# Kernel optimization log

Hardware: AMD Instinct MI355X
Metric: run time of the kernel (lower is better)

The kernel has to match this reference:

```python
import jax, jax.numpy as jnp
import numpy as np

N = 4096      # num_nodes (also node feature dim)
E = 32768     # num_edges
EMB = 8       # embedding_dim


def setup_inputs() -> dict:
    key = jax.random.key(0)
    ks = jax.random.split(key, 12)
    s = lambda fan_in: 1.0 / np.sqrt(fan_in)
    return {
        "x": jax.random.normal(ks[0], (N, N), dtype=jnp.float32),
        "edge_index": jax.random.randint(ks[1], (2, E), 0, N, dtype=jnp.int64),
        "edge_weight": jax.random.uniform(ks[2], (E,), dtype=jnp.float32),
        # GCNConv linear (PyG Linear, weight [out,in]) + bias
        "gcn_w": jax.random.normal(ks[3], (N, N), dtype=jnp.float32) * s(N),
        "gcn_b": jnp.zeros((N,), dtype=jnp.float32),
        # Wq: Linear(N -> E)
        "wq_w": jax.random.normal(ks[4], (E, N), dtype=jnp.float32) * s(N),
        "wq_b": jax.random.normal(ks[5], (E,), dtype=jnp.float32) * s(N),
        # edge embedding table [E, EMB]
        "emb": jax.random.normal(ks[6], (E, EMB), dtype=jnp.float32),
        # WF: Linear(N+EMB -> 1)
        "wf_w": jax.random.normal(ks[7], (1, N + EMB), dtype=jnp.float32) * s(N + EMB),
        "wf_b": jax.random.normal(ks[8], (1,), dtype=jnp.float32) * s(N + EMB),
    }


def reference(x, edge_index, edge_weight, gcn_w, gcn_b, wq_w, wq_b, emb, wf_w, wf_b):
    n = x.shape[0]
    row, col = edge_index[0], edge_index[1]
    # --- GCNConv: add self loops (weight 1.0), symmetric normalization ---
    loop = jnp.arange(n)
    row_f = jnp.concatenate([row, loop])
    col_f = jnp.concatenate([col, loop])
    w_f = jnp.concatenate([edge_weight, jnp.ones((n,), dtype=x.dtype)])
    deg = jax.ops.segment_sum(w_f, col_f, num_segments=n)          # weighted in-degree
    dis = jnp.where(deg > 0, jax.lax.rsqrt(deg), 0.0)              # deg^{-1/2}, 0 for isolated
    norm = dis[row_f] * w_f * dis[col_f]                           # [E+N]
    h = x @ gcn_w.T                                                # linear transform first (as PyG)
    agg = jax.ops.segment_sum(norm[:, None] * h[row_f], col_f, num_segments=n)
    H1 = jnp.tanh(agg + gcn_b)                                     # [N, N]
    # --- dense head ---
    H2 = jnp.tanh(H1 @ wq_w.T + wq_b)                              # [N, E]
    H2_t = H2.T                                                    # [E, N]
    feat = jnp.concatenate([H2_t, emb], axis=1)                    # [E, N+EMB]
    F_hat = (feat @ wf_w.T + wf_b)[:, 0]                           # [E]
    return F_hat
```

## Files before the change

kernel.cpp:

```cpp
#include <hip/hip_runtime.h>
#include <hip/hip_bf16.h>

#define NN 4096
#define NE 32768
#define NEMB 8

typedef __bf16 bf16x8 __attribute__((ext_vector_type(8)));
typedef float  f32x4  __attribute__((ext_vector_type(4)));

__device__ __forceinline__ unsigned short f2bf(float f) {
  union { float f; unsigned int u; } v; v.f = f;
  return (unsigned short)((v.u + 0x7FFFu + ((v.u >> 16) & 1u)) >> 16);
}
__device__ __forceinline__ float b2f(unsigned short u) {
  union { unsigned int u; float f; } v; v.u = ((unsigned int)u) << 16;
  return v.f;
}

__global__ void k_f2bf(const float* __restrict__ in, unsigned short* __restrict__ out, long n8) {
  long i = (long)blockIdx.x * blockDim.x + threadIdx.x;
  long stride = (long)gridDim.x * blockDim.x;
  for (long j = i; j < n8; j += stride) {
    const float* p = in + j * 8;
    float4 a = *(const float4*)p;
    float4 b = *(const float4*)(p + 4);
    union { unsigned short u[8]; uint4 v; } o;
    o.u[0] = f2bf(a.x); o.u[1] = f2bf(a.y); o.u[2] = f2bf(a.z); o.u[3] = f2bf(a.w);
    o.u[4] = f2bf(b.x); o.u[5] = f2bf(b.y); o.u[6] = f2bf(b.z); o.u[7] = f2bf(b.w);
    *(uint4*)(out + j * 8) = o.v;
  }
}

__global__ void k_deg_init(float* deg) { deg[blockIdx.x * 256 + threadIdx.x] = 1.0f; }

__global__ void k_edge_accum(const int* __restrict__ ei, const float* __restrict__ ew,
                             float* deg, int* cnt) {
  int e = blockIdx.x * 256 + threadIdx.x;
  if (e >= NE) return;
  int c = ei[NE + e];
  atomicAdd(&deg[c], ew[e]);
  atomicAdd(&cnt[c], 1);
}

__global__ void k_dis(const float* __restrict__ deg, float* __restrict__ dis) {
  int i = blockIdx.x * 256 + threadIdx.x;
  float d = deg[i];
  dis[i] = d > 0.f ? rsqrtf(d) : 0.f;
}

__global__ void k_scan(const int* __restrict__ cnt, int* __restrict__ starts) {
  __shared__ int sh[1024];
  int tid = threadIdx.x;
  int base = tid * 4;
  int v[4]; int sum = 0;
  for (int i = 0; i < 4; i++) { v[i] = cnt[base + i]; sum += v[i]; }
  sh[tid] = sum;
  __syncthreads();
  for (int offd = 1; offd < 1024; offd <<= 1) {
    int t = (tid >= offd) ? sh[tid - offd] : 0;
    __syncthreads();
    sh[tid] += t;
    __syncthreads();
  }
  int run = sh[tid] - sum;
  for (int i = 0; i < 4; i++) { starts[base + i] = run; run += v[i]; }
}

__global__ void k_fill(const int* __restrict__ ei, const int* __restrict__ starts,
                       int* cursor, int* csr_e) {
  int e = blockIdx.x * 256 + threadIdx.x;
  if (e >= NE) return;
  int c = ei[NE + e];
  int pos = atomicAdd(&cursor[c], 1);
  csr_e[starts[c] + pos] = e;
}

__global__ void k_sortnorm(const int* __restrict__ ei, const float* __restrict__ ew,
                           const int* __restrict__ starts, const int* __restrict__ cnt,
                           const float* __restrict__ dis,
                           int* csr_e, int* __restrict__ csr_row, float* __restrict__ csr_nrm) {
  int n = blockIdx.x * 256 + threadIdx.x;
  if (n >= NN) return;
  int s = starts[n], c = cnt[n];
  for (int i = 1; i < c; i++) {
    int key = csr_e[s + i]; int j = i - 1;
    while (j >= 0 && csr_e[s + j] > key) { csr_e[s + j + 1] = csr_e[s + j]; j--; }
    csr_e[s + j + 1] = key;
  }
  float dn = dis[n];
  for (int i = 0; i < c; i++) {
    int e = csr_e[s + i];
    int r = ei[e];
    csr_row[s + i] = r;
    csr_nrm[s + i] = dis[r] * ew[e] * dn;
  }
}

__global__ __launch_bounds__(256) void k_agg(
    const unsigned short* __restrict__ h, const float* __restrict__ dis,
    const int* __restrict__ starts, const int* __restrict__ cnt,
    const int* __restrict__ csr_row, const float* __restrict__ csr_nrm,
    const float* __restrict__ gcn_b, unsigned short* __restrict__ H1b) {
  int n = blockIdx.x;
  int tid = threadIdx.x;
  float dn = dis[n];
  float sw = dn * dn;
  float acc[16];
  const unsigned short* hn = h + (size_t)n * NN;
  #pragma unroll
  for (int i = 0; i < 16; i++) { int f = tid + i * 256; acc[i] = sw * b2f(hn[f]) + gcn_b[f]; }
  int s = starts[n], c = cnt[n];
  __shared__ int   s_row[64];
  __shared__ float s_nrm[64];
  for (int base = 0; base < c; base += 64) {
    int m = min(64, c - base);
    __syncthreads();
    if (tid < m) { s_row[tid] = csr_row[s + base + tid]; s_nrm[tid] = csr_nrm[s + base + tid]; }
    __syncthreads();
    for (int j = 0; j < m; j++) {
      const unsigned short* hr = h + (size_t)s_row[j] * NN;
      float wgt = s_nrm[j];
      #pragma unroll
      for (int i = 0; i < 16; i++) acc[i] += wgt * b2f(hr[tid + i * 256]);
    }
  }
  #pragma unroll
  for (int i = 0; i < 16; i++)
    H1b[(size_t)n * NN + tid + i * 256] = f2bf(tanhf(acc[i]));
}

__device__ __forceinline__ void gload16(const void* g, void* l) {
  __builtin_amdgcn_global_load_lds(
      (const __attribute__((address_space(1))) unsigned int*)g,
      (__attribute__((address_space(3))) unsigned int*)l, 16, 0, 0);
}

#define BARX() do { __builtin_amdgcn_sched_barrier(0); __builtin_amdgcn_s_barrier(); __builtin_amdgcn_sched_barrier(0); } while (0)
#define VMC(n) do { asm volatile("s_waitcnt vmcnt(" #n ")" ::: "memory"); } while (0)


#define STAGE(buf, mat, kk, tk) do { \
    size_t off_ = (size_t)(tk) * 64 + (kk) * 32; \
    gload16((mat ? gB0 : gA0) + off_, &LDS[buf][mat][kk][c0][0]); \
    gload16((mat ? gB1 : gA1) + off_, &LDS[buf][mat][kk][c0 + 1][0]); \
  } while (0)

#define LDA4(dst, buf, kk, q) do { \
    const unsigned short* b_ = &LDS[buf][0][kk][wr * 8 + (q) * 4][0] + aoff; \
    dst[0] = *(const bf16x8*)(b_); \
    dst[1] = *(const bf16x8*)(b_ + 512); \
    dst[2] = *(const bf16x8*)(b_ + 1024); \
    dst[3] = *(const bf16x8*)(b_ + 1536); \
  } while (0)

#define LDB4(dst, buf, kk) do { \
    const unsigned short* b_ = &LDS[buf][1][kk][wc * 4][0] + aoff; \
    dst[0] = *(const bf16x8*)(b_); \
    dst[1] = *(const bf16x8*)(b_ + 512); \
    dst[2] = *(const bf16x8*)(b_ + 1024); \
    dst[3] = *(const bf16x8*)(b_ + 1536); \
  } while (0)

#define MMA_RDA(q, bufA, kkA, qA) do { \
    __builtin_amdgcn_s_setprio(1); \
    _Pragma("unroll") \
    for (int mf_ = 0; mf_ < 4; mf_++) { \
      _Pragma("unroll") \
      for (int nf_ = 0; nf_ < 4; nf_++) \
        acc[(q) * 4 + mf_][nf_] = __builtin_amdgcn_mfma_f32_16x16x32_bf16(av[mf_], bv[nf_], acc[(q) * 4 + mf_][nf_], 0, 0, 0); \
      const unsigned short* a_ = &LDS[bufA][0][kkA][wr * 8 + (qA) * 4 + mf_][0] + aoff; \
      av[mf_] = *(const bf16x8*)(a_); \
    } \
    __builtin_amdgcn_s_setprio(0); \
  } while (0)

#define MMA16(q) do { \
    __builtin_amdgcn_s_setprio(1); \
    _Pragma("unroll") \
    for (int mf_ = 0; mf_ < 4; mf_++) \
      _Pragma("unroll") \
      for (int nf_ = 0; nf_ < 4; nf_++) \
        acc[(q) * 4 + mf_][nf_] = __builtin_amdgcn_mfma_f32_16x16x32_bf16(av[mf_], bv[nf_], acc[(q) * 4 + mf_][nf_], 0, 0, 0); \
    __builtin_amdgcn_s_setprio(0); \
  } while (0)

template<bool FUSED>
__global__ __launch_bounds__(512, 2) void gemm8(
    const unsigned short* __restrict__ A,
    const unsigned short* __restrict__ B,
    int N, int K, int nRb,
    void* __restrict__ outP,
    const float* __restrict__ colBias,
    const float* __restrict__ rowW,
    float* __restrict__ P) {
  __shared__ unsigned short LDS[2][2][2][16][512];

  const int nwg = gridDim.x, n8 = nwg >> 3;
  const int bid = blockIdx.x;
  const int swz = (bid & 7) * n8 + (bid >> 3);
  const int rb = swz % nRb, cb = swz / nRb;
  const int row0 = rb * 256, col0 = cb * 256;

  const int tid = threadIdx.x;
  const int w = tid >> 6, l = tid & 63;
  const int wr = w >> 2, wc = w & 3;
  const int l15 = l & 15, kl = l >> 4;

  const int c0 = w * 2;
  const int pq = l >> 2;
  const int pc = (l & 3) ^ ((l >> 3) & 3);
  const unsigned short* gA0 = A + (size_t)(row0 + c0 * 16 + pq) * K + pc * 8;
  const unsigned short* gA1 = gA0 + (size_t)16 * K;
  const unsigned short* gB0 = B + (size_t)(col0 + c0 * 16 + pq) * K + pc * 8;
  const unsigned short* gB1 = gB0 + (size_t)16 * K;

  const int aoff = l15 * 32 + ((kl ^ ((l >> 1) & 3)) << 3);

  f32x4 acc[8][4];
  #pragma unroll
  for (int m = 0; m < 8; m++)
    #pragma unroll
    for (int n = 0; n < 4; n++)
      acc[m][n] = f32x4{0.f, 0.f, 0.f, 0.f};

  bf16x8 av[4], bv[4];

  STAGE(0, 0, 0, 0); STAGE(0, 1, 0, 0); STAGE(0, 0, 1, 0); STAGE(0, 1, 1, 0);
  STAGE(1, 0, 0, 1); STAGE(1, 1, 0, 1);
  VMC(4);
  BARX();

  const int NIT = K >> 7;
  for (int i = 0; i < NIT; i++) {
    const int ta = 2 * i, tb = 2 * i + 1;
    const bool mid = (i < NIT - 1);
    if (i) {
      MMA_RDA(1, 0, 0, 0);
      LDB4(bv, 0, 0);
    } else {
      LDA4(av, 0, 0, 0);
      LDB4(bv, 0, 0);
    }
    STAGE(1, 0, 1, tb);
    MMA_RDA(0, 0, 0, 1);
    STAGE(1, 1, 1, tb);
    VMC(8);
    BARX();
    MMA_RDA(1, 0, 1, 0);
    LDB4(bv, 0, 1);
    if (mid) STAGE(0, 0, 0, ta + 2);
    MMA_RDA(0, 0, 1, 1);
    if (mid) STAGE(0, 1, 0, ta + 2);
    if (mid) VMC(8); else VMC(4);
    BARX();
    MMA_RDA(1, 1, 0, 0);
    LDB4(bv, 1, 0);
    if (mid) STAGE(0, 0, 1, ta + 2);
    MMA_RDA(0, 1, 0, 1);
    if (mid) STAGE(0, 1, 1, ta + 2);
    if (mid) VMC(8); else VMC(0);
    BARX();
    MMA_RDA(1, 1, 1, 0);
    LDB4(bv, 1, 1);
    if (mid) STAGE(1, 0, 0, tb + 2);
    MMA_RDA(0, 1, 1, 1);
    if (mid) STAGE(1, 1, 0, tb + 2);
    if (mid) VMC(8);
    BARX();
  }
  MMA16(1);

  if (!FUSED) {
    unsigned short* outB = (unsigned short*)outP;
    #pragma unroll
    for (int mf = 0; mf < 8; mf++)
      #pragma unroll
      for (int nf = 0; nf < 4; nf++) {
        int row = row0 + wr * 128 + mf * 16 + kl * 4;
        int col = col0 + wc * 64 + nf * 16 + l15;
        unsigned short* o = outB + (size_t)row * N + col;
        #pragma unroll
        for (int r = 0; r < 4; r++) o[(size_t)r * N] = f2bf(acc[mf][nf][r]);
      }
  } else {
    #pragma unroll
    for (int nf = 0; nf < 4; nf++) {
      int col = col0 + wc * 64 + nf * 16 + l15;
      float bias = colBias[col];
      float s = 0.f;
      #pragma unroll
      for (int mf = 0; mf < 8; mf++) {
        int rbase = row0 + wr * 128 + mf * 16 + kl * 4;
        #pragma unroll
        for (int r = 0; r < 4; r++)
          s += rowW[rbase + r] * tanhf(acc[mf][nf][r] + bias);
      }
      s += __shfl_xor(s, 16, 64);
      s += __shfl_xor(s, 32, 64);
      if (l < 16) P[(size_t)(rb * 2 + wr) * N + col] = s;
    }
  }
}

__global__ void k_final(const float* __restrict__ P, const float* __restrict__ emb,
                        const float* __restrict__ wf, const float* __restrict__ wfb,
                        float* __restrict__ out) {
  int e = blockIdx.x * 256 + threadIdx.x;
  float s = 0.f;
  for (int r = 0; r < 32; r++) s += P[(size_t)r * NE + e];
  float c = wfb[0];
  #pragma unroll
  for (int k = 0; k < NEMB; k++) c += emb[e * NEMB + k] * wf[NN + k];
  out[e] = s + c;
}

extern "C" void kernel_launch(void* const* d_in, const int* in_sizes, int n_in,
                              void* d_out, int out_size, void* d_ws, size_t ws_size,
                              hipStream_t stream) {
  const float* x    = (const float*)d_in[0];
  const int*   ei   = (const int*)d_in[1];
  const float* ew   = (const float*)d_in[2];
  const float* gcnw = (const float*)d_in[3];
  const float* gcnb = (const float*)d_in[4];
  const float* wqw  = (const float*)d_in[5];
  const float* wqb  = (const float*)d_in[6];
  const float* emb  = (const float*)d_in[7];
  const float* wfw  = (const float*)d_in[8];
  const float* wfb  = (const float*)d_in[9];
  float* out = (float*)d_out;

  char* ws = (char*)d_ws;
  size_t off = 0;
  auto alloc = [&](size_t b) { char* p = ws + off; off += (b + 255) & ~(size_t)255; return p; };

  unsigned short* wq16  = (unsigned short*)alloc((size_t)NE * NN * 2);
  unsigned short* h     = (unsigned short*)alloc((size_t)NN * NN * 2);
  unsigned short* x16   = (unsigned short*)alloc((size_t)NN * NN * 2);
  unsigned short* w16   = (unsigned short*)alloc((size_t)NN * NN * 2);
  unsigned short* h1b   = (unsigned short*)alloc((size_t)NN * NN * 2);
  float* deg    = (float*)alloc(NN * 4);
  float* dis    = (float*)alloc(NN * 4);
  int*   cnt    = (int*)alloc(NN * 4);
  int*   cursor = (int*)alloc(NN * 4);
  int*   starts = (int*)alloc(NN * 4);
  int*   csr_e  = (int*)alloc(NE * 4);
  int*   csr_row= (int*)alloc(NE * 4);
  float* csr_nrm= (float*)alloc(NE * 4);
  float* P      = (float*)alloc((size_t)32 * NE * 4);

  hipMemsetAsync(cnt, 0, NN * 4 * 2, stream);

  k_deg_init<<<NN / 256, 256, 0, stream>>>(deg);
  k_edge_accum<<<NE / 256, 256, 0, stream>>>(ei, ew, deg, cnt);
  k_dis<<<NN / 256, 256, 0, stream>>>(deg, dis);
  k_scan<<<1, 1024, 0, stream>>>(cnt, starts);
  k_fill<<<NE / 256, 256, 0, stream>>>(ei, starts, cursor, csr_e);
  k_sortnorm<<<NN / 256, 256, 0, stream>>>(ei, ew, starts, cnt, dis, csr_e, csr_row, csr_nrm);

  k_f2bf<<<1024, 256, 0, stream>>>(x, x16, (long)NN * NN / 8);
  k_f2bf<<<1024, 256, 0, stream>>>(gcnw, w16, (long)NN * NN / 8);
  k_f2bf<<<2048, 256, 0, stream>>>(wqw, wq16, (long)NE * NN / 8);

  gemm8<false><<<16 * 16, 512, 0, stream>>>(x16, w16, NN, NN, 16, h, nullptr, nullptr, nullptr);

  k_agg<<<NN, 256, 0, stream>>>(h, dis, starts, cnt, csr_row, csr_nrm, gcnb, h1b);

  gemm8<true><<<16 * 128, 512, 0, stream>>>(h1b, wq16, NE, NN, 16, nullptr, wqb, wfw, P);

  k_final<<<NE / 256, 256, 0, stream>>>(P, emb, wfw, wfb, out);
}
```

Measured before the change: 1.370 ms.

## Restructure GEMM main loop into paired MMA phases with interleaved next-tile LDS reads

Replaces the per-half MMA_RDA macros with a PAIR macro. It computes both 4-row halves of a k-slice and, during the second half, reads the next k-slice's A and B fragments from LDS. Global staging is issued in pairs before each phase, and the vmcnt waits change from 8 to 4. The goal is to hide the LDS read latency of the B fragments behind MFMA work and to simplify the barrier schedule. In exchange, fewer global loads can be in flight at each wait, and the LDS buffer reuse ordering becomes riskier.

```diff
diff --git a/kernel.cpp b/kernel.cpp
--- a/kernel.cpp
+++ b/kernel.cpp
@@ -161,26 +161,26 @@
     dst[3] = *(const bf16x8*)(b_ + 1536); \
   } while (0)
 
-#define MMA_RDA(q, bufA, kkA, qA) do { \
+#define PAIR(bufC, kkC, bufN, kkN, doRef) do { \
     __builtin_amdgcn_s_setprio(1); \
     _Pragma("unroll") \
     for (int mf_ = 0; mf_ < 4; mf_++) { \
       _Pragma("unroll") \
       for (int nf_ = 0; nf_ < 4; nf_++) \
-        acc[(q) * 4 + mf_][nf_] = __builtin_amdgcn_mfma_f32_16x16x32_bf16(av[mf_], bv[nf_], acc[(q) * 4 + mf_][nf_], 0, 0, 0); \
-      const unsigned short* a_ = &LDS[bufA][0][kkA][wr * 8 + (qA) * 4 + mf_][0] + aoff; \
-      av[mf_] = *(const bf16x8*)(a_); \
+        acc[mf_][nf_] = __builtin_amdgcn_mfma_f32_16x16x32_bf16(av[mf_], bv[nf_], acc[mf_][nf_], 0, 0, 0); \
+      av[mf_] = *(const bf16x8*)(&LDS[bufC][0][kkC][wr * 8 + 4 + mf_][0] + aoff); \
     } \
-    __builtin_amdgcn_s_setprio(0); \
-  } while (0)
-
-#define MMA16(q) do { \
-    __builtin_amdgcn_s_setprio(1); \
     _Pragma("unroll") \
-    for (int mf_ = 0; mf_ < 4; mf_++) \
+    for (int nf_ = 0; nf_ < 4; nf_++) { \
       _Pragma("unroll") \
-      for (int nf_ = 0; nf_ < 4; nf_++) \
-        acc[(q) * 4 + mf_][nf_] = __builtin_amdgcn_mfma_f32_16x16x32_bf16(av[mf_], bv[nf_], acc[(q) * 4 + mf_][nf_], 0, 0, 0); \
+      for (int mf_ = 0; mf_ < 4; mf_++) { \
+        acc[4 + mf_][nf_] = __builtin_amdgcn_mfma_f32_16x16x32_bf16(av[mf_], bv[nf_], acc[4 + mf_][nf_], 0, 0, 0); \
+        if ((doRef) && nf_ == 3) \
+          av[mf_] = *(const bf16x8*)(&LDS[bufN][0][kkN][wr * 8 + mf_][0] + aoff); \
+      } \
+      if (doRef) \
+        bv[nf_] = *(const bf16x8*)(&LDS[bufN][1][kkN][wc * 4 + nf_][0] + aoff); \
+    } \
     __builtin_amdgcn_s_setprio(0); \
   } while (0)
 
@@ -229,46 +229,32 @@
   STAGE(1, 0, 0, 1); STAGE(1, 1, 0, 1);
   VMC(4);
   BARX();
+  LDA4(av, 0, 0, 0); LDB4(bv, 0, 0);
 
   const int NIT = K >> 7;
   for (int i = 0; i < NIT; i++) {
     const int ta = 2 * i, tb = 2 * i + 1;
     const bool mid = (i < NIT - 1);
-    if (i) {
-      MMA_RDA(1, 0, 0, 0);
-      LDB4(bv, 0, 0);
+    STAGE(1, 0, 1, tb); STAGE(1, 1, 1, tb);
+    PAIR(0, 0, 0, 1, true);
+    VMC(4); BARX();
+    if (mid) { STAGE(0, 0, 0, ta + 2); STAGE(0, 1, 0, ta + 2); }
+    PAIR(0, 1, 1, 0, true);
+    if (mid) VMC(4); else VMC(0);
+    BARX();
+    if (mid) { STAGE(0, 0, 1, ta + 2); STAGE(0, 1, 1, ta + 2); }
+    PAIR(1, 0, 1, 1, true);
+    if (mid) VMC(4);
+    BARX();
+    if (mid) {
+      STAGE(1, 0, 0, tb + 2); STAGE(1, 1, 0, tb + 2);
+      PAIR(1, 1, 0, 0, true);
+      VMC(4);
     } else {
-      LDA4(av, 0, 0, 0);
-      LDB4(bv, 0, 0);
+      PAIR(1, 1, 0, 0, false);
     }
-    STAGE(1, 0, 1, tb);
-    MMA_RDA(0, 0, 0, 1);
-    STAGE(1, 1, 1, tb);
-    VMC(8);
     BARX();
-    MMA_RDA(1, 0, 1, 0);
-    LDB4(bv, 0, 1);
-    if (mid) STAGE(0, 0, 0, ta + 2);
-    MMA_RDA(0, 0, 1, 1);
-    if (mid) STAGE(0, 1, 0, ta + 2);
-    if (mid) VMC(8); else VMC(4);
-    BARX();
-    MMA_RDA(1, 1, 0, 0);
-    LDB4(bv, 1, 0);
-    if (mid) STAGE(0, 0, 1, ta + 2);
-    MMA_RDA(0, 1, 0, 1);
-    if (mid) STAGE(0, 1, 1, ta + 2);
-    if (mid) VMC(8); else VMC(0);
-    BARX();
-    MMA_RDA(1, 1, 1, 0);
-    LDB4(bv, 1, 1);
-    if (mid) STAGE(1, 0, 0, tb + 2);
-    MMA_RDA(0, 1, 1, 1);
-    if (mid) STAGE(1, 1, 0, tb + 2);
-    if (mid) VMC(8);
-    BARX();
-  }
-  MMA16(1);
+  }
 
   if (!FUSED) {
     unsigned short* outB = (unsigned short*)outP;
```

Result: slower. 4.616 ms (+236.8%).
